# Kernel tuning notes

Measured on AMD Instinct MI355X. Metric: run time of the kernel, lower is better.

Reference implementation:

```python
import jax, jax.numpy as jnp
import numpy as np

B, N, FN, FE = 8, 256, 64, 64  # batch, nodes, node feat, edge feat


def gnn_layer(A, x, e, We, be, Wn, bn):
    # A: [B,N,N] float mask, x: [B,N,Fn], e: [B,N,N,Fe_in]
    b, n, fn = x.shape
    xi = jnp.broadcast_to(x[:, :, None, :], (b, n, n, fn))  # sender feats
    xj = jnp.broadcast_to(x[:, None, :, :], (b, n, n, fn))  # receiver feats
    h = jnp.concatenate([xi, xj, e], axis=-1)               # [B,N,N,2Fn+Fe]
    e_new = jax.nn.relu(jnp.einsum('bijk,kf->bijf', h, We) + be) * A[..., None]
    deg = jnp.clip(jnp.sum(A, axis=2), 1.0, None)           # [B,N]
    agg = jnp.sum(e_new, axis=2) / deg[..., None]           # mean over neighbors
    x_new = jax.nn.relu(jnp.concatenate([x, agg], axis=-1) @ Wn + bn)
    return x_new, e_new


def setup_inputs() -> dict:
    key = jax.random.key(0)
    ks = jax.random.split(key, 20)
    s = 0.05
    inp = {
        'edge_index': jax.random.randint(ks[0], (B, N, N), 0, 2, dtype=jnp.int32),
        'x': jax.random.normal(ks[1], (B, N, FN), dtype=jnp.float32),
        'edge_attr': jax.random.normal(ks[2], (B, N, N, FE), dtype=jnp.float32),
    }
    # 3 GNN layers: edge-update MLP (2Fn+Fe -> Fe) and node-update (Fn+Fe -> Fn)
    for l in range(3):
        inp[f'We{l}'] = jax.random.normal(ks[3 + 4 * l], (2 * FN + FE, FE), jnp.float32) * s
        inp[f'be{l}'] = jnp.zeros((FE,), jnp.float32)
        inp[f'Wn{l}'] = jax.random.normal(ks[4 + 4 * l], (FN + FE, FN), jnp.float32) * s
        inp[f'bn{l}'] = jnp.zeros((FN,), jnp.float32)
    # spectral-norm MLP head: Fe -> Fe -> Fe -> 1
    inp['W1'] = jax.random.normal(ks[15], (FE, FE), jnp.float32) * s
    inp['b1'] = jnp.zeros((FE,), jnp.float32)
    inp['W2'] = jax.random.normal(ks[16], (FE, FE), jnp.float32) * s
    inp['b2'] = jnp.zeros((FE,), jnp.float32)
    inp['W3'] = jax.random.normal(ks[17], (FE, 1), jnp.float32) * s
    inp['b3'] = jnp.zeros((1,), jnp.float32)
    return inp


def reference(edge_index, x, edge_attr,
              We0, be0, Wn0, bn0,
              We1, be1, Wn1, bn1,
              We2, be2, Wn2, bn2,
              W1, b1, W2, b2, W3, b3):
    A = edge_index.astype(jnp.float32)
    x = x.astype(jnp.float32)
    # layer 0 updates both nodes and edges
    x1, e = gnn_layer(A, x, edge_attr, We0, be0, Wn0, bn0)
    # middle layer(s): node output discarded (as in original forward)
    _, e = gnn_layer(A, x1, e, We1, be1, Wn1, bn1)
    # last layer
    _, edges = gnn_layer(A, x1, e, We2, be2, Wn2, bn2)
    # end == 'edge_mean'
    v = jnp.mean(edges, axis=(1, 2))  # [B, FE]
    h = jax.nn.relu(v @ W1 + b1)
    h = jax.nn.relu(h @ W2 + b2)
    out = h @ W3 + b3                  # [B, 1]
    return jnp.squeeze(out, axis=-1)   # [B]
```

## Files before the change

kernel.cpp:

```cpp
#include <hip/hip_runtime.h>

#define BB 8
#define NN 256
#define FF 64

typedef float f32x4 __attribute__((ext_vector_type(4)));
typedef short s16x8 __attribute__((ext_vector_type(8)));
typedef unsigned short u16;

#define MFMA_BF16(a, b, c) __builtin_amdgcn_mfma_f32_16x16x32_bf16(a, b, c, 0, 0, 0)

__device__ inline u16 f2bf(float x) {
    unsigned u = __float_as_uint(x);
    u += 0x7FFFu + ((u >> 16) & 1u);
    return (u16)(u >> 16);
}
__device__ inline float bf2f(u16 h) { return __uint_as_float(((unsigned)h) << 16); }

__device__ inline s16x8 cvt_a(float4 v0, float4 v1) {
    s16x8 a;
    a[0] = (short)f2bf(v0.x); a[1] = (short)f2bf(v0.y);
    a[2] = (short)f2bf(v0.z); a[3] = (short)f2bf(v0.w);
    a[4] = (short)f2bf(v1.x); a[5] = (short)f2bf(v1.y);
    a[6] = (short)f2bf(v1.z); a[7] = (short)f2bf(v1.w);
    return a;
}

__global__ __launch_bounds__(256) void wprep_kernel(
    const float* __restrict__ We0, const float* __restrict__ We1,
    const float* __restrict__ We2, u16* __restrict__ wimg)
{
    const float* src =
        (blockIdx.x == 0 ? We0 : (blockIdx.x == 1 ? We1 : We2)) + 2 * FF * FF;
    u16* hi = wimg + blockIdx.x * 8192;
    u16* lo = hi + 4096;
    for (int idx = threadIdx.x; idx < 4096; idx += 256) {
        const int f = idx >> 6, rem = idx & 63, cs = rem >> 3, j = rem & 7;
        const int k = ((cs ^ (f & 7)) << 3) | j;
        const float wv = src[k * FF + f];
        const u16 h = f2bf(wv);
        hi[idx] = h;
        lo[idx] = f2bf(wv - bf2f(h));
    }
}

__global__ __launch_bounds__(256) void pq_kernel(
    const float* __restrict__ x, const float* __restrict__ We,
    const float* __restrict__ be, float* __restrict__ P, float* __restrict__ Q,
    float* __restrict__ agg)
{
    const int rl = threadIdx.x >> 6, f = threadIdx.x & 63;
    const int r = blockIdx.x * 4 + rl;
    __shared__ float xs[4][FF];
    xs[rl][f] = x[r * FF + f];
    agg[r * FF + f] = 0.f;
    __syncthreads();
    float p = be[f], q = 0.f;
#pragma unroll
    for (int k = 0; k < FF; ++k) {
        const float xv = xs[rl][k];
        p = fmaf(xv, We[k * FF + f], p);
        q = fmaf(xv, We[(FF + k) * FF + f], q);
    }
    P[r * FF + f] = p;
    Q[r * FF + f] = q;
}

__global__ __launch_bounds__(256) void edge0_kernel(
    const float* __restrict__ e_in, const u16* __restrict__ whi,
    const u16* __restrict__ wlo, const float* __restrict__ P,
    const float* __restrict__ Q, const int* __restrict__ A,
    float* __restrict__ e_out, float* __restrict__ agg)
{
    __shared__ u16 Whl[4096], Wll[4096];
    __shared__ float Al[128], Pl[64];

    const int tid = threadIdx.x;
    const int bt  = blockIdx.x;
    const int bi  = bt >> 1;
    const int b   = bi >> 8;
    const int j0  = (bt & 1) << 7;

#pragma unroll
    for (int m = 0; m < 2; ++m) {
        ((uint4*)Whl)[tid + 256 * m] = ((const uint4*)whi)[tid + 256 * m];
        ((uint4*)Wll)[tid + 256 * m] = ((const uint4*)wlo)[tid + 256 * m];
    }
    if (tid < 128) Al[tid] = (float)A[bi * NN + j0 + tid];
    if (tid < 64)  Pl[tid] = P[bi * FF + tid];

    const int w = tid >> 6, lane = tid & 63;
    const int quad = lane >> 4, l15 = lane & 15, l7 = lane & 7;
    const int e_base = 32 * w;

    const float* erow = e_in + ((size_t)bi * NN + j0) * FF;

    s16x8 afr[2][2];
#pragma unroll
    for (int ks = 0; ks < 2; ++ks)
#pragma unroll
        for (int et = 0; et < 2; ++et) {
            const float* p = erow + (e_base + et * 16 + l15) * FF + ks * 32 + quad * 8;
            afr[ks][et] = cvt_a(*(const float4*)p, *(const float4*)(p + 4));
        }

    float qv[2][4][4];
    const float* Qb = Q + (size_t)b * NN * FF;
#pragma unroll
    for (int et = 0; et < 2; ++et)
#pragma unroll
        for (int ft = 0; ft < 4; ++ft)
#pragma unroll
            for (int r = 0; r < 4; ++r)
                qv[et][ft][r] =
                    Qb[(j0 + e_base + et * 16 + quad * 4 + r) * FF + ft * 16 + l15];

    __syncthreads();

    f32x4 acc[2][4];
#pragma unroll
    for (int et = 0; et < 2; ++et)
#pragma unroll
        for (int ft = 0; ft < 4; ++ft) acc[et][ft] = (f32x4){0.f, 0.f, 0.f, 0.f};

#pragma unroll
    for (int ks = 0; ks < 2; ++ks)
#pragma unroll
        for (int ft = 0; ft < 4; ++ft) {
            const int f  = ft * 16 + l15;
            const int ca = (ks * 4 + quad) ^ l7;
            const s16x8 bh = *(const s16x8*)&Whl[f * 64 + ca * 8];
            const s16x8 bl = *(const s16x8*)&Wll[f * 64 + ca * 8];
#pragma unroll
            for (int et = 0; et < 2; ++et) {
                acc[et][ft] = MFMA_BF16(afr[ks][et], bh, acc[et][ft]);
                acc[et][ft] = MFMA_BF16(afr[ks][et], bl, acc[et][ft]);
            }
        }

    float psum[4] = {0.f, 0.f, 0.f, 0.f};
#pragma unroll
    for (int et = 0; et < 2; ++et)
#pragma unroll
        for (int ft = 0; ft < 4; ++ft)
#pragma unroll
            for (int r = 0; r < 4; ++r) {
                const int el = e_base + et * 16 + quad * 4 + r;
                const int f  = ft * 16 + l15;
                const float val = acc[et][ft][r] + Pl[f] + qv[et][ft][r];
                const float rv  = fmaxf(val, 0.f) * Al[el];
                e_out[((size_t)bi * NN + j0 + el) * FF + f] = rv;
                psum[ft] += rv;
            }
#pragma unroll
    for (int ft = 0; ft < 4; ++ft) {
        psum[ft] += __shfl_down(psum[ft], 32);
        psum[ft] += __shfl_down(psum[ft], 16);
    }
    if (lane < 16) {
#pragma unroll
        for (int ft = 0; ft < 4; ++ft)
            atomicAdd(&agg[bi * FF + ft * 16 + l15], psum[ft]);
    }
}

__global__ __launch_bounds__(256) void nodepq_kernel(
    const float* __restrict__ x, const float* __restrict__ agg,
    const int* __restrict__ A,
    const float* __restrict__ Wn, const float* __restrict__ bn,
    const float* __restrict__ We1, const float* __restrict__ be1,
    const float* __restrict__ We2, const float* __restrict__ be2,
    float* __restrict__ P1, float* __restrict__ Q1,
    float* __restrict__ P2, float* __restrict__ Q2, float* __restrict__ v)
{
    const int rl = threadIdx.x >> 6, f = threadIdx.x & 63;
    const int r = blockIdx.x * 4 + rl;
    __shared__ float s[4][2 * FF];
    __shared__ float x1s[4][FF];

    float da = (float)A[r * NN + f] + (float)A[r * NN + f + 64] +
               (float)A[r * NN + f + 128] + (float)A[r * NN + f + 192];
#pragma unroll
    for (int off = 32; off > 0; off >>= 1) da += __shfl_down(da, off, 64);
    const float deg = fmaxf(__shfl(da, 0, 64), 1.0f);

    s[rl][f]      = x[r * FF + f];
    s[rl][FF + f] = agg[r * FF + f] / deg;
    if (blockIdx.x == 0) {
        v[threadIdx.x] = 0.f;
        v[256 + threadIdx.x] = 0.f;
    }
    __syncthreads();
    float a = bn[f];
#pragma unroll
    for (int k = 0; k < 2 * FF; ++k) a = fmaf(s[rl][k], Wn[k * FF + f], a);
    x1s[rl][f] = fmaxf(a, 0.f);
    __syncthreads();
    float p1 = be1[f], q1 = 0.f, p2 = be2[f], q2 = 0.f;
#pragma unroll
    for (int k = 0; k < FF; ++k) {
        const float xv = x1s[rl][k];
        p1 = fmaf(xv, We1[k * FF + f], p1);
        q1 = fmaf(xv, We1[(FF + k) * FF + f], q1);
        p2 = fmaf(xv, We2[k * FF + f], p2);
        q2 = fmaf(xv, We2[(FF + k) * FF + f], q2);
    }
    P1[r * FF + f] = p1;  Q1[r * FF + f] = q1;
    P2[r * FF + f] = p2;  Q2[r * FF + f] = q2;
}

__global__ __launch_bounds__(256) void edge12_kernel(
    const float* __restrict__ e_in,
    const u16* __restrict__ w1hi, const u16* __restrict__ w1lo,
    const u16* __restrict__ w2hi, const u16* __restrict__ w2lo,
    const float* __restrict__ P1, const float* __restrict__ Q1,
    const float* __restrict__ P2, const float* __restrict__ Q2,
    const int* __restrict__ A, float* __restrict__ v)
{
    __shared__ u16 W1h[4096], W1l[4096], W2h[4096], W2l[4096];
    __shared__ u16 E2[128 * 64];
    __shared__ float Al[128], Pl1[64], Pl2[64], red[64];

    const int tid = threadIdx.x;
    const int bt  = blockIdx.x;
    const int bi  = bt >> 1;
    const int b   = bi >> 8;
    const int j0  = (bt & 1) << 7;

#pragma unroll
    for (int m = 0; m < 2; ++m) {
        ((uint4*)W1h)[tid + 256 * m] = ((const uint4*)w1hi)[tid + 256 * m];
        ((uint4*)W1l)[tid + 256 * m] = ((const uint4*)w1lo)[tid + 256 * m];
        ((uint4*)W2h)[tid + 256 * m] = ((const uint4*)w2hi)[tid + 256 * m];
        ((uint4*)W2l)[tid + 256 * m] = ((const uint4*)w2lo)[tid + 256 * m];
    }
    if (tid < 128) Al[tid] = (float)A[bi * NN + j0 + tid];
    if (tid < 64) {
        Pl1[tid] = P1[bi * FF + tid];
        Pl2[tid] = P2[bi * FF + tid];
        red[tid] = 0.f;
    }

    const int w = tid >> 6, lane = tid & 63;
    const int quad = lane >> 4, l15 = lane & 15, l7 = lane & 7;
    const int e_base = 32 * w;

    const float* erow = e_in + ((size_t)bi * NN + j0) * FF;

    s16x8 afr[2][2];
#pragma unroll
    for (int ks = 0; ks < 2; ++ks)
#pragma unroll
        for (int et = 0; et < 2; ++et) {
            const float* p = erow + (e_base + et * 16 + l15) * FF + ks * 32 + quad * 8;
            afr[ks][et] = cvt_a(*(const float4*)p, *(const float4*)(p + 4));
        }

    float qv[2][4][4];
    {
        const float* Q1b = Q1 + (size_t)b * NN * FF;
#pragma unroll
        for (int et = 0; et < 2; ++et)
#pragma unroll
            for (int ft = 0; ft < 4; ++ft)
#pragma unroll
                for (int r = 0; r < 4; ++r)
                    qv[et][ft][r] =
                        Q1b[(j0 + e_base + et * 16 + quad * 4 + r) * FF + ft * 16 + l15];
    }

    __syncthreads();

    f32x4 acc[2][4];
#pragma unroll
    for (int et = 0; et < 2; ++et)
#pragma unroll
        for (int ft = 0; ft < 4; ++ft) acc[et][ft] = (f32x4){0.f, 0.f, 0.f, 0.f};

#pragma unroll
    for (int ks = 0; ks < 2; ++ks)
#pragma unroll
        for (int ft = 0; ft < 4; ++ft) {
            const int f  = ft * 16 + l15;
            const int ca = (ks * 4 + quad) ^ l7;
            const s16x8 bh = *(const s16x8*)&W1h[f * 64 + ca * 8];
            const s16x8 bl = *(const s16x8*)&W1l[f * 64 + ca * 8];
#pragma unroll
            for (int et = 0; et < 2; ++et) {
                acc[et][ft] = MFMA_BF16(afr[ks][et], bh, acc[et][ft]);
                acc[et][ft] = MFMA_BF16(afr[ks][et], bl, acc[et][ft]);
            }
        }

#pragma unroll
    for (int et = 0; et < 2; ++et)
#pragma unroll
        for (int ft = 0; ft < 4; ++ft)
#pragma unroll
            for (int r = 0; r < 4; ++r) {
                const int el = e_base + et * 16 + quad * 4 + r;
                const int f  = ft * 16 + l15;
                const float val = acc[et][ft][r] + Pl1[f] + qv[et][ft][r];
                const float rv  = fmaxf(val, 0.f) * Al[el];
                const int c  = f >> 3;
                const int cs = c ^ (el & 7);
                E2[el * 64 + cs * 8 + l7] = f2bf(rv);
            }

    {
        const float* Q2b = Q2 + (size_t)b * NN * FF;
#pragma unroll
        for (int et = 0; et < 2; ++et)
#pragma unroll
            for (int ft = 0; ft < 4; ++ft)
#pragma unroll
                for (int r = 0; r < 4; ++r)
                    qv[et][ft][r] =
                        Q2b[(j0 + e_base + et * 16 + quad * 4 + r) * FF + ft * 16 + l15];
    }

    __syncthreads();

#pragma unroll
    for (int et = 0; et < 2; ++et)
#pragma unroll
        for (int ft = 0; ft < 4; ++ft) acc[et][ft] = (f32x4){0.f, 0.f, 0.f, 0.f};

#pragma unroll
    for (int ks = 0; ks < 2; ++ks) {
        s16x8 a2[2];
#pragma unroll
        for (int et = 0; et < 2; ++et) {
            const int e  = e_base + et * 16 + l15;
            const int ca = (ks * 4 + quad) ^ l7;
            a2[et] = *(const s16x8*)&E2[e * 64 + ca * 8];
        }
#pragma unroll
        for (int ft = 0; ft < 4; ++ft) {
            const int f  = ft * 16 + l15;
            const int ca = (ks * 4 + quad) ^ l7;
            const s16x8 bh = *(const s16x8*)&W2h[f * 64 + ca * 8];
            const s16x8 bl = *(const s16x8*)&W2l[f * 64 + ca * 8];
#pragma unroll
            for (int et = 0; et < 2; ++et) {
                acc[et][ft] = MFMA_BF16(a2[et], bh, acc[et][ft]);
                acc[et][ft] = MFMA_BF16(a2[et], bl, acc[et][ft]);
            }
        }
    }

    float psum[4] = {0.f, 0.f, 0.f, 0.f};
#pragma unroll
    for (int et = 0; et < 2; ++et)
#pragma unroll
        for (int ft = 0; ft < 4; ++ft)
#pragma unroll
            for (int r = 0; r < 4; ++r) {
                const int el = e_base + et * 16 + quad * 4 + r;
                const int f  = ft * 16 + l15;
                const float val = acc[et][ft][r] + Pl2[f] + qv[et][ft][r];
                psum[ft] += fmaxf(val, 0.f) * Al[el];
            }
#pragma unroll
    for (int ft = 0; ft < 4; ++ft) {
        psum[ft] += __shfl_down(psum[ft], 32);
        psum[ft] += __shfl_down(psum[ft], 16);
    }
    if (lane < 16) {
#pragma unroll
        for (int ft = 0; ft < 4; ++ft)
            atomicAdd(&red[ft * 16 + l15], psum[ft]);
    }
    __syncthreads();
    if (tid < 64) atomicAdd(&v[b * FF + tid], red[tid]);
}

__global__ __launch_bounds__(64) void head_kernel(
    const float* __restrict__ vsum, const float* __restrict__ W1,
    const float* __restrict__ b1, const float* __restrict__ W2,
    const float* __restrict__ b2, const float* __restrict__ W3,
    const float* __restrict__ b3, float* __restrict__ out)
{
    const int f = threadIdx.x;
    __shared__ float hv[BB][FF];
    __shared__ float h1[BB][FF];
#pragma unroll
    for (int b = 0; b < BB; ++b) hv[b][f] = vsum[b * FF + f] * (1.0f / 65536.0f);
    __syncthreads();
#pragma unroll
    for (int b = 0; b < BB; ++b) {
        float acc = b1[f];
#pragma unroll
        for (int k = 0; k < FF; ++k) acc = fmaf(hv[b][k], W1[k * FF + f], acc);
        h1[b][f] = fmaxf(acc, 0.f);
    }
    __syncthreads();
#pragma unroll
    for (int b = 0; b < BB; ++b) {
        float acc = b2[f];
#pragma unroll
        for (int k = 0; k < FF; ++k) acc = fmaf(h1[b][k], W2[k * FF + f], acc);
        hv[b][f] = fmaxf(acc, 0.f);
    }
    __syncthreads();
#pragma unroll
    for (int b = 0; b < BB; ++b) {
        float p = hv[b][f] * W3[f];
#pragma unroll
        for (int off = 32; off > 0; off >>= 1) p += __shfl_down(p, off);
        if (f == 0) out[b] = p + b3[0];
    }
}

extern "C" void kernel_launch(void* const* d_in, const int* in_sizes, int n_in,
                              void* d_out, int out_size, void* d_ws, size_t ws_size,
                              hipStream_t stream)
{
    const int*   A      = (const int*)d_in[0];
    const float* x      = (const float*)d_in[1];
    float*       e_attr = (float*)d_in[2];

    const float* We0 = (const float*)d_in[3];
    const float* be0 = (const float*)d_in[4];
    const float* Wn0 = (const float*)d_in[5];
    const float* bn0 = (const float*)d_in[6];
    const float* We1 = (const float*)d_in[7];
    const float* be1 = (const float*)d_in[8];
    const float* We2 = (const float*)d_in[11];
    const float* be2 = (const float*)d_in[12];
    const float* W1 = (const float*)d_in[15];
    const float* b1 = (const float*)d_in[16];
    const float* W2 = (const float*)d_in[17];
    const float* b2 = (const float*)d_in[18];
    const float* W3 = (const float*)d_in[19];
    const float* b3 = (const float*)d_in[20];
    float* out = (float*)d_out;
    (void)in_sizes; (void)n_in; (void)out_size; (void)ws_size;

    const int R = BB * NN;
    float* P1  = (float*)d_ws;
    float* Q1  = P1 + R * FF;
    float* P2  = Q1 + R * FF;
    float* Q2  = P2 + R * FF;
    float* agg = Q2 + R * FF;
    float* v   = agg + R * FF;
    u16*  wimg = (u16*)(v + 512);

    const int EB = 2 * R;

    wprep_kernel<<<3, 256, 0, stream>>>(We0, We1, We2, wimg);
    pq_kernel<<<R / 4, 256, 0, stream>>>(x, We0, be0, P1, Q1, agg);
    edge0_kernel<<<EB, 256, 0, stream>>>(e_attr, wimg, wimg + 4096, P1, Q1, A,
                                         e_attr, agg);
    nodepq_kernel<<<R / 4, 256, 0, stream>>>(x, agg, A, Wn0, bn0, We1, be1,
                                             We2, be2, P1, Q1, P2, Q2, v);
    edge12_kernel<<<EB, 256, 0, stream>>>(e_attr,
                                          wimg + 8192, wimg + 12288,
                                          wimg + 16384, wimg + 20480,
                                          P1, Q1, P2, Q2, A, v);
    head_kernel<<<1, 64, 0, stream>>>(v, W1, b1, W2, b2, W3, b3, out);
}
```

Measured before the change: 361.7 us.

## Store intermediate edges as bf16, batch edge tiles per block, fold weight prep into pq

Layer-0 edge outputs are now written as bf16 into the existing edge buffer, reusing the same 256-byte row stride. edge12 reads these bf16 values directly as MFMA operands, which cuts the global traffic for the intermediate edge tensor roughly in half and removes an fp32-to-bf16 conversion. Each block now handles several edge tiles (T0/T12), so the LDS weight image is loaded fewer times. The MFMA operands are swapped so each lane holds four contiguous features, which allows vectorized P/Q loads and ushort4 stores. The weight-prep kernel is merged into pq_kernel to save a launch, edge12 uses a per-warp E2 buffer so block syncs are no longer needed, and atomics are accumulated across the tiles before they are issued. The risk is that the weight image from pq blocks 0-2 must be ready before edge0 runs, which holds because of stream order.

New measurement: 485.9 us. +34.3%, slower.

```diff
diff --git a/kernel.cpp b/kernel.cpp
--- a/kernel.cpp
+++ b/kernel.cpp
@@ -3,6 +3,9 @@
 #define BB 8
 #define NN 256
 #define FF 64
+#define T0  4
+#define T12 4
+#define E2S 72
 
 typedef float f32x4 __attribute__((ext_vector_type(4)));
 typedef short s16x8 __attribute__((ext_vector_type(8)));
@@ -17,43 +20,42 @@
 }
 __device__ inline float bf2f(u16 h) { return __uint_as_float(((unsigned)h) << 16); }
 
-__device__ inline s16x8 cvt_a(float4 v0, float4 v1) {
-    s16x8 a;
-    a[0] = (short)f2bf(v0.x); a[1] = (short)f2bf(v0.y);
-    a[2] = (short)f2bf(v0.z); a[3] = (short)f2bf(v0.w);
-    a[4] = (short)f2bf(v1.x); a[5] = (short)f2bf(v1.y);
-    a[6] = (short)f2bf(v1.z); a[7] = (short)f2bf(v1.w);
-    return a;
-}
-
-__global__ __launch_bounds__(256) void wprep_kernel(
-    const float* __restrict__ We0, const float* __restrict__ We1,
-    const float* __restrict__ We2, u16* __restrict__ wimg)
-{
-    const float* src =
-        (blockIdx.x == 0 ? We0 : (blockIdx.x == 1 ? We1 : We2)) + 2 * FF * FF;
-    u16* hi = wimg + blockIdx.x * 8192;
-    u16* lo = hi + 4096;
-    for (int idx = threadIdx.x; idx < 4096; idx += 256) {
-        const int f = idx >> 6, rem = idx & 63, cs = rem >> 3, j = rem & 7;
-        const int k = ((cs ^ (f & 7)) << 3) | j;
-        const float wv = src[k * FF + f];
-        const u16 h = f2bf(wv);
-        hi[idx] = h;
-        lo[idx] = f2bf(wv - bf2f(h));
-    }
+__device__ inline s16x8 cvt8(f32x4 a, f32x4 b) {
+    s16x8 r;
+    r[0] = (short)f2bf(a[0]); r[1] = (short)f2bf(a[1]);
+    r[2] = (short)f2bf(a[2]); r[3] = (short)f2bf(a[3]);
+    r[4] = (short)f2bf(b[0]); r[5] = (short)f2bf(b[1]);
+    r[6] = (short)f2bf(b[2]); r[7] = (short)f2bf(b[3]);
+    return r;
 }
 
 __global__ __launch_bounds__(256) void pq_kernel(
     const float* __restrict__ x, const float* __restrict__ We,
     const float* __restrict__ be, float* __restrict__ P, float* __restrict__ Q,
-    float* __restrict__ agg)
+    float* __restrict__ agg,
+    const float* __restrict__ We0, const float* __restrict__ We1,
+    const float* __restrict__ We2, u16* __restrict__ wimg)
 {
     const int rl = threadIdx.x >> 6, f = threadIdx.x & 63;
     const int r = blockIdx.x * 4 + rl;
     __shared__ float xs[4][FF];
     xs[rl][f] = x[r * FF + f];
     agg[r * FF + f] = 0.f;
+
+    if (blockIdx.x < 3) {
+        const float* src =
+            (blockIdx.x == 0 ? We0 : (blockIdx.x == 1 ? We1 : We2)) + 2 * FF * FF;
+        u16* hi = wimg + blockIdx.x * 8192;
+        u16* lo = hi + 4096;
+        for (int idx = threadIdx.x; idx < 4096; idx += 256) {
+            const int ff = idx >> 6, rem = idx & 63, cs = rem >> 3, j = rem & 7;
+            const int k = ((cs ^ (ff & 7)) << 3) | j;
+            const float wv = src[k * FF + ff];
+            const u16 h = f2bf(wv);
+            hi[idx] = h;
+            lo[idx] = f2bf(wv - bf2f(h));
+        }
+    }
     __syncthreads();
     float p = be[f], q = 0.f;
 #pragma unroll
@@ -67,100 +69,117 @@
 }
 
 __global__ __launch_bounds__(256) void edge0_kernel(
-    const float* __restrict__ e_in, const u16* __restrict__ whi,
-    const u16* __restrict__ wlo, const float* __restrict__ P,
-    const float* __restrict__ Q, const int* __restrict__ A,
-    float* __restrict__ e_out, float* __restrict__ agg)
-{
-    __shared__ u16 Whl[4096], Wll[4096];
-    __shared__ float Al[128], Pl[64];
-
+    const float* __restrict__ e_in, u16* __restrict__ e1_out,
+    const u16* __restrict__ wimg, const float* __restrict__ P,
+    const float* __restrict__ Q, const int* __restrict__ Adj,
+    float* __restrict__ agg)
+{
+    __shared__ u16 Wh[4096], Wl[4096];
     const int tid = threadIdx.x;
-    const int bt  = blockIdx.x;
-    const int bi  = bt >> 1;
-    const int b   = bi >> 8;
-    const int j0  = (bt & 1) << 7;
-
 #pragma unroll
     for (int m = 0; m < 2; ++m) {
-        ((uint4*)Whl)[tid + 256 * m] = ((const uint4*)whi)[tid + 256 * m];
-        ((uint4*)Wll)[tid + 256 * m] = ((const uint4*)wlo)[tid + 256 * m];
-    }
-    if (tid < 128) Al[tid] = (float)A[bi * NN + j0 + tid];
-    if (tid < 64)  Pl[tid] = P[bi * FF + tid];
+        ((uint4*)Wh)[tid + 256 * m] = ((const uint4*)wimg)[tid + 256 * m];
+        ((uint4*)Wl)[tid + 256 * m] = ((const uint4*)(wimg + 4096))[tid + 256 * m];
+    }
+    __syncthreads();
 
     const int w = tid >> 6, lane = tid & 63;
     const int quad = lane >> 4, l15 = lane & 15, l7 = lane & 7;
-    const int e_base = 32 * w;
-
-    const float* erow = e_in + ((size_t)bi * NN + j0) * FF;
-
-    s16x8 afr[2][2];
-#pragma unroll
-    for (int ks = 0; ks < 2; ++ks)
+    const int e0 = 32 * w + l15;
+
+#pragma unroll
+    for (int tt = 0; tt < T0; ++tt) {
+        const int bt = blockIdx.x * T0 + tt;
+        const int bi = bt >> 1, b = bi >> 8;
+        const int j0 = (bt & 1) << 7;
+
+        f32x4 ef[2][2][2];
+        const float* erow = e_in + ((size_t)bi * NN + j0) * FF;
+#pragma unroll
+        for (int ks = 0; ks < 2; ++ks)
+#pragma unroll
+            for (int et = 0; et < 2; ++et) {
+                const float* p = erow + (size_t)(e0 + 16 * et) * FF + ks * 32 + quad * 8;
+                ef[ks][et][0] = *(const f32x4*)p;
+                ef[ks][et][1] = *(const f32x4*)(p + 4);
+            }
+
+        float av[2];
+#pragma unroll
+        for (int et = 0; et < 2; ++et)
+            av[et] = (float)Adj[bi * NN + j0 + e0 + 16 * et];
+        f32x4 pv[4];
+#pragma unroll
+        for (int ft = 0; ft < 4; ++ft)
+            pv[ft] = *(const f32x4*)(P + bi * FF + ft * 16 + quad * 4);
+        f32x4 qv[2][4];
+        const float* Qb = Q + ((size_t)b * NN + j0) * FF;
+#pragma unroll
+        for (int et = 0; et < 2; ++et)
+#pragma unroll
+            for (int ft = 0; ft < 4; ++ft)
+                qv[et][ft] = *(const f32x4*)(Qb + (size_t)(e0 + 16 * et) * FF +
+                                             ft * 16 + quad * 4);
+
+        f32x4 acc[2][4];
+#pragma unroll
+        for (int et = 0; et < 2; ++et)
+#pragma unroll
+            for (int ft = 0; ft < 4; ++ft) acc[et][ft] = (f32x4){0.f, 0.f, 0.f, 0.f};
+
+#pragma unroll
+        for (int ks = 0; ks < 2; ++ks) {
+            s16x8 efr[2];
+#pragma unroll
+            for (int et = 0; et < 2; ++et) efr[et] = cvt8(ef[ks][et][0], ef[ks][et][1]);
+#pragma unroll
+            for (int ft = 0; ft < 4; ++ft) {
+                const int off = (16 * ft + l15) * 64 + (((ks * 4 + quad) ^ l7) << 3);
+                const s16x8 ah = *(const s16x8*)&Wh[off];
+                const s16x8 al = *(const s16x8*)&Wl[off];
+#pragma unroll
+                for (int et = 0; et < 2; ++et) {
+                    acc[et][ft] = MFMA_BF16(ah, efr[et], acc[et][ft]);
+                    acc[et][ft] = MFMA_BF16(al, efr[et], acc[et][ft]);
+                }
+            }
+        }
+
+        float sac[4][4];
+#pragma unroll
+        for (int ft = 0; ft < 4; ++ft)
+#pragma unroll
+            for (int r = 0; r < 4; ++r) sac[ft][r] = 0.f;
 #pragma unroll
         for (int et = 0; et < 2; ++et) {
-            const float* p = erow + (e_base + et * 16 + l15) * FF + ks * 32 + quad * 8;
-            afr[ks][et] = cvt_a(*(const float4*)p, *(const float4*)(p + 4));
-        }
-
-    float qv[2][4][4];
-    const float* Qb = Q + (size_t)b * NN * FF;
-#pragma unroll
-    for (int et = 0; et < 2; ++et)
+            const size_t erow_g = (size_t)bi * NN + j0 + e0 + 16 * et;
+#pragma unroll
+            for (int ft = 0; ft < 4; ++ft) {
+                float rr[4];
+#pragma unroll
+                for (int r = 0; r < 4; ++r) {
+                    const float val = acc[et][ft][r] + pv[ft][r] + qv[et][ft][r];
+                    rr[r] = fmaxf(val, 0.f) * av[et];
+                    sac[ft][r] += rr[r];
+                }
+                ushort4 st;
+                st.x = f2bf(rr[0]); st.y = f2bf(rr[1]);
+                st.z = f2bf(rr[2]); st.w = f2bf(rr[3]);
+                *(ushort4*)(e1_out + erow_g * 128 + ft * 16 + quad * 4) = st;
+            }
+        }
 #pragma unroll
         for (int ft = 0; ft < 4; ++ft)
 #pragma unroll
-            for (int r = 0; r < 4; ++r)
-                qv[et][ft][r] =
-                    Qb[(j0 + e_base + et * 16 + quad * 4 + r) * FF + ft * 16 + l15];
-
-    __syncthreads();
-
-    f32x4 acc[2][4];
-#pragma unroll
-    for (int et = 0; et < 2; ++et)
-#pragma unroll
-        for (int ft = 0; ft < 4; ++ft) acc[et][ft] = (f32x4){0.f, 0.f, 0.f, 0.f};
-
-#pragma unroll
-    for (int ks = 0; ks < 2; ++ks)
-#pragma unroll
-        for (int ft = 0; ft < 4; ++ft) {
-            const int f  = ft * 16 + l15;
-            const int ca = (ks * 4 + quad) ^ l7;
-            const s16x8 bh = *(const s16x8*)&Whl[f * 64 + ca * 8];
-            const s16x8 bl = *(const s16x8*)&Wll[f * 64 + ca * 8];
-#pragma unroll
-            for (int et = 0; et < 2; ++et) {
-                acc[et][ft] = MFMA_BF16(afr[ks][et], bh, acc[et][ft]);
-                acc[et][ft] = MFMA_BF16(afr[ks][et], bl, acc[et][ft]);
-            }
-        }
-
-    float psum[4] = {0.f, 0.f, 0.f, 0.f};
-#pragma unroll
-    for (int et = 0; et < 2; ++et)
-#pragma unroll
-        for (int ft = 0; ft < 4; ++ft)
-#pragma unroll
             for (int r = 0; r < 4; ++r) {
-                const int el = e_base + et * 16 + quad * 4 + r;
-                const int f  = ft * 16 + l15;
-                const float val = acc[et][ft][r] + Pl[f] + qv[et][ft][r];
-                const float rv  = fmaxf(val, 0.f) * Al[el];
-                e_out[((size_t)bi * NN + j0 + el) * FF + f] = rv;
-                psum[ft] += rv;
-            }
-#pragma unroll
-    for (int ft = 0; ft < 4; ++ft) {
-        psum[ft] += __shfl_down(psum[ft], 32);
-        psum[ft] += __shfl_down(psum[ft], 16);
-    }
-    if (lane < 16) {
-#pragma unroll
-        for (int ft = 0; ft < 4; ++ft)
-            atomicAdd(&agg[bi * FF + ft * 16 + l15], psum[ft]);
+                float s = sac[ft][r];
+                s += __shfl_xor(s, 1, 16);
+                s += __shfl_xor(s, 2, 16);
+                s += __shfl_xor(s, 4, 16);
+                s += __shfl_xor(s, 8, 16);
+                if (l15 == 0)
+                    atomicAdd(&agg[bi * FF + ft * 16 + quad * 4 + r], s);
+            }
     }
 }
 
@@ -210,169 +229,161 @@
 }
 
 __global__ __launch_bounds__(256) void edge12_kernel(
-    const float* __restrict__ e_in,
-    const u16* __restrict__ w1hi, const u16* __restrict__ w1lo,
-    const u16* __restrict__ w2hi, const u16* __restrict__ w2lo,
+    const u16* __restrict__ e1,
+    const u16* __restrict__ w1img, const u16* __restrict__ w2img,
     const float* __restrict__ P1, const float* __restrict__ Q1,
     const float* __restrict__ P2, const float* __restrict__ Q2,
-    const int* __restrict__ A, float* __restrict__ v)
+    const int* __restrict__ Adj, float* __restrict__ v)
 {
     __shared__ u16 W1h[4096], W1l[4096], W2h[4096], W2l[4096];
-    __shared__ u16 E2[128 * 64];
-    __shared__ float Al[128], Pl1[64], Pl2[64], red[64];
-
+    __shared__ u16 E2[4][32 * E2S];
     const int tid = threadIdx.x;
-    const int bt  = blockIdx.x;
-    const int bi  = bt >> 1;
-    const int b   = bi >> 8;
-    const int j0  = (bt & 1) << 7;
-
 #pragma unroll
     for (int m = 0; m < 2; ++m) {
-        ((uint4*)W1h)[tid + 256 * m] = ((const uint4*)w1hi)[tid + 256 * m];
-        ((uint4*)W1l)[tid + 256 * m] = ((const uint4*)w1lo)[tid + 256 * m];
-        ((uint4*)W2h)[tid + 256 * m] = ((const uint4*)w2hi)[tid + 256 * m];
-        ((uint4*)W2l)[tid + 256 * m] = ((const uint4*)w2lo)[tid + 256 * m];
-    }
-    if (tid < 128) Al[tid] = (float)A[bi * NN + j0 + tid];
-    if (tid < 64) {
-        Pl1[tid] = P1[bi * FF + tid];
-        Pl2[tid] = P2[bi * FF + tid];
-        red[tid] = 0.f;
-    }
+        ((uint4*)W1h)[tid + 256 * m] = ((const uint4*)w1img)[tid + 256 * m];
+        ((uint4*)W1l)[tid + 256 * m] = ((const uint4*)(w1img + 4096))[tid + 256 * m];
+        ((uint4*)W2h)[tid + 256 * m] = ((const uint4*)w2img)[tid + 256 * m];
+        ((uint4*)W2l)[tid + 256 * m] = ((const uint4*)(w2img + 4096))[tid + 256 * m];
+    }
+    __syncthreads();
 
     const int w = tid >> 6, lane = tid & 63;
     const int quad = lane >> 4, l15 = lane & 15, l7 = lane & 7;
-    const int e_base = 32 * w;
-
-    const float* erow = e_in + ((size_t)bi * NN + j0) * FF;
-
-    s16x8 afr[2][2];
-#pragma unroll
-    for (int ks = 0; ks < 2; ++ks)
+    const int e0 = 32 * w + l15;
+    u16* E2w = E2[w];
+    const int b = (blockIdx.x * T12) >> 9;
+
+    float vac[4][4];
+#pragma unroll
+    for (int ft = 0; ft < 4; ++ft)
+#pragma unroll
+        for (int r = 0; r < 4; ++r) vac[ft][r] = 0.f;
+
+#pragma unroll
+    for (int tt = 0; tt < T12; ++tt) {
+        const int bt = blockIdx.x * T12 + tt;
+        const int bi = bt >> 1;
+        const int j0 = (bt & 1) << 7;
+
+        s16x8 bfr[2][2];
+#pragma unroll
+        for (int ks = 0; ks < 2; ++ks)
+#pragma unroll
+            for (int et = 0; et < 2; ++et)
+                bfr[ks][et] = *(const s16x8*)(e1 +
+                    ((size_t)bi * NN + j0 + e0 + 16 * et) * 128 + ks * 32 + quad * 8);
+
+        float av[2];
+#pragma unroll
+        for (int et = 0; et < 2; ++et)
+            av[et] = (float)Adj[bi * NN + j0 + e0 + 16 * et];
+        f32x4 pv[4];
+#pragma unroll
+        for (int ft = 0; ft < 4; ++ft)
+            pv[ft] = *(const f32x4*)(P1 + bi * FF + ft * 16 + quad * 4);
+        f32x4 qv[2][4];
+        const float* Q1b = Q1 + ((size_t)b * NN + j0) * FF;
+#pragma unroll
+        for (int et = 0; et < 2; ++et)
+#pragma unroll
+            for (int ft = 0; ft < 4; ++ft)
+                qv[et][ft] = *(const f32x4*)(Q1b + (size_t)(e0 + 16 * et) * FF +
+                                             ft * 16 + quad * 4);
+
+        f32x4 acc[2][4];
+#pragma unroll
+        for (int et = 0; et < 2; ++et)
+#pragma unroll
+            for (int ft = 0; ft < 4; ++ft) acc[et][ft] = (f32x4){0.f, 0.f, 0.f, 0.f};
+#pragma unroll
+        for (int ks = 0; ks < 2; ++ks)
+#pragma unroll
+            for (int ft = 0; ft < 4; ++ft) {
+                const int off = (16 * ft + l15) * 64 + (((ks * 4 + quad) ^ l7) << 3);
+                const s16x8 ah = *(const s16x8*)&W1h[off];
+                const s16x8 al = *(const s16x8*)&W1l[off];
+#pragma unroll
+                for (int et = 0; et < 2; ++et) {
+                    acc[et][ft] = MFMA_BF16(ah, bfr[ks][et], acc[et][ft]);
+                    acc[et][ft] = MFMA_BF16(al, bfr[ks][et], acc[et][ft]);
+                }
+            }
+
 #pragma unroll
         for (int et = 0; et < 2; ++et) {
-            const float* p = erow + (e_base + et * 16 + l15) * FF + ks * 32 + quad * 8;
-            afr[ks][et] = cvt_a(*(const float4*)p, *(const float4*)(p + 4));
-        }
-
-    float qv[2][4][4];
-    {
-        const float* Q1b = Q1 + (size_t)b * NN * FF;
+            const int erow_l = (16 * et + l15) * E2S;
+#pragma unroll
+            for (int ft = 0; ft < 4; ++ft) {
+                float rr[4];
+#pragma unroll
+                for (int r = 0; r < 4; ++r) {
+                    const float val = acc[et][ft][r] + pv[ft][r] + qv[et][ft][r];
+                    rr[r] = fmaxf(val, 0.f) * av[et];
+                }
+                ushort4 st;
+                st.x = f2bf(rr[0]); st.y = f2bf(rr[1]);
+                st.z = f2bf(rr[2]); st.w = f2bf(rr[3]);
+                *(ushort4*)&E2w[erow_l + ft * 16 + quad * 4] = st;
+            }
+        }
+
+#pragma unroll
+        for (int ft = 0; ft < 4; ++ft)
+            pv[ft] = *(const f32x4*)(P2 + bi * FF + ft * 16 + quad * 4);
+        const float* Q2b = Q2 + ((size_t)b * NN + j0) * FF;
 #pragma unroll
         for (int et = 0; et < 2; ++et)
 #pragma unroll
             for (int ft = 0; ft < 4; ++ft)
-#pragma unroll
-                for (int r = 0; r < 4; ++r)
-                    qv[et][ft][r] =
-                        Q1b[(j0 + e_base + et * 16 + quad * 4 + r) * FF + ft * 16 + l15];
-    }
-
-    __syncthreads();
-
-    f32x4 acc[2][4];
-#pragma unroll
-    for (int et = 0; et < 2; ++et)
-#pragma unroll
-        for (int ft = 0; ft < 4; ++ft) acc[et][ft] = (f32x4){0.f, 0.f, 0.f, 0.f};
-
-#pragma unroll
-    for (int ks = 0; ks < 2; ++ks)
-#pragma unroll
-        for (int ft = 0; ft < 4; ++ft) {
-            const int f  = ft * 16 + l15;
-            const int ca = (ks * 4 + quad) ^ l7;
-            const s16x8 bh = *(const s16x8*)&W1h[f * 64 + ca * 8];
-            const s16x8 bl = *(const s16x8*)&W1l[f * 64 + ca * 8];
-#pragma unroll
-            for (int et = 0; et < 2; ++et) {
-                acc[et][ft] = MFMA_BF16(afr[ks][et], bh, acc[et][ft]);
-                acc[et][ft] = MFMA_BF16(afr[ks][et], bl, acc[et][ft]);
-            }
-        }
-
-#pragma unroll
-    for (int et = 0; et < 2; ++et)
-#pragma unroll
-        for (int ft = 0; ft < 4; ++ft)
-#pragma unroll
-            for (int r = 0; r < 4; ++r) {
-                const int el = e_base + et * 16 + quad * 4 + r;
-                const int f  = ft * 16 + l15;
-                const float val = acc[et][ft][r] + Pl1[f] + qv[et][ft][r];
-                const float rv  = fmaxf(val, 0.f) * Al[el];
-                const int c  = f >> 3;
-                const int cs = c ^ (el & 7);
-                E2[el * 64 + cs * 8 + l7] = f2bf(rv);
-            }
-
-    {
-        const float* Q2b = Q2 + (size_t)b * NN * FF;
+                qv[et][ft] = *(const f32x4*)(Q2b + (size_t)(e0 + 16 * et) * FF +
+                                             ft * 16 + quad * 4);
+
+#pragma unroll
+        for (int et = 0; et < 2; ++et)
+#pragma unroll
+            for (int ft = 0; ft < 4; ++ft) acc[et][ft] = (f32x4){0.f, 0.f, 0.f, 0.f};
+#pragma unroll
+        for (int ks = 0; ks < 2; ++ks) {
+            s16x8 e2f[2];
+#pragma unroll
+            for (int et = 0; et < 2; ++et)
+                e2f[et] = *(const s16x8*)&E2w[(16 * et + l15) * E2S + ks * 32 + quad * 8];
+#pragma unroll
+            for (int ft = 0; ft < 4; ++ft) {
+                const int off = (16 * ft + l15) * 64 + (((ks * 4 + quad) ^ l7) << 3);
+                const s16x8 ah = *(const s16x8*)&W2h[off];
+                const s16x8 al = *(const s16x8*)&W2l[off];
+#pragma unroll
+                for (int et = 0; et < 2; ++et) {
+                    acc[et][ft] = MFMA_BF16(ah, e2f[et], acc[et][ft]);
+                    acc[et][ft] = MFMA_BF16(al, e2f[et], acc[et][ft]);
+                }
+            }
+        }
+
 #pragma unroll
         for (int et = 0; et < 2; ++et)
 #pragma unroll
             for (int ft = 0; ft < 4; ++ft)
 #pragma unroll
-                for (int r = 0; r < 4; ++r)
-                    qv[et][ft][r] =
-                        Q2b[(j0 + e_base + et * 16 + quad * 4 + r) * FF + ft * 16 + l15];
-    }
-
-    __syncthreads();
-
-#pragma unroll
-    for (int et = 0; et < 2; ++et)
-#pragma unroll
-        for (int ft = 0; ft < 4; ++ft) acc[et][ft] = (f32x4){0.f, 0.f, 0.f, 0.f};
-
-#pragma unroll
-    for (int ks = 0; ks < 2; ++ks) {
-        s16x8 a2[2];
-#pragma unroll
-        for (int et = 0; et < 2; ++et) {
-            const int e  = e_base + et * 16 + l15;
-            const int ca = (ks * 4 + quad) ^ l7;
-            a2[et] = *(const s16x8*)&E2[e * 64 + ca * 8];
-        }
-#pragma unroll
-        for (int ft = 0; ft < 4; ++ft) {
-            const int f  = ft * 16 + l15;
-            const int ca = (ks * 4 + quad) ^ l7;
-            const s16x8 bh = *(const s16x8*)&W2h[f * 64 + ca * 8];
-            const s16x8 bl = *(const s16x8*)&W2l[f * 64 + ca * 8];
-#pragma unroll
-            for (int et = 0; et < 2; ++et) {
-                acc[et][ft] = MFMA_BF16(a2[et], bh, acc[et][ft]);
-                acc[et][ft] = MFMA_BF16(a2[et], bl, acc[et][ft]);
-            }
-        }
-    }
-
-    float psum[4] = {0.f, 0.f, 0.f, 0.f};
-#pragma unroll
-    for (int et = 0; et < 2; ++et)
-#pragma unroll
-        for (int ft = 0; ft < 4; ++ft)
-#pragma unroll
-            for (int r = 0; r < 4; ++r) {
-                const int el = e_base + et * 16 + quad * 4 + r;
-                const int f  = ft * 16 + l15;
-                const float val = acc[et][ft][r] + Pl2[f] + qv[et][ft][r];
-                psum[ft] += fmaxf(val, 0.f) * Al[el];
-            }
-#pragma unroll
-    for (int ft = 0; ft < 4; ++ft) {
-        psum[ft] += __shfl_down(psum[ft], 32);
-        psum[ft] += __shfl_down(psum[ft], 16);
-    }
-    if (lane < 16) {
-#pragma unroll
-        for (int ft = 0; ft < 4; ++ft)
-            atomicAdd(&red[ft * 16 + l15], psum[ft]);
-    }
-    __syncthreads();
-    if (tid < 64) atomicAdd(&v[b * FF + tid], red[tid]);
+                for (int r = 0; r < 4; ++r) {
+                    const float val = acc[et][ft][r] + pv[ft][r] + qv[et][ft][r];
+                    vac[ft][r] += fmaxf(val, 0.f) * av[et];
+                }
+    }
+
+#pragma unroll
+    for (int ft = 0; ft < 4; ++ft)
+#pragma unroll
+        for (int r = 0; r < 4; ++r) {
+            float s = vac[ft][r];
+            s += __shfl_xor(s, 1, 16);
+            s += __shfl_xor(s, 2, 16);
+            s += __shfl_xor(s, 4, 16);
+            s += __shfl_xor(s, 8, 16);
+            if (l15 == 0)
+                atomicAdd(&v[b * FF + ft * 16 + quad * 4 + r], s);
+        }
 }
 
 __global__ __launch_bounds__(64) void head_kernel(
@@ -446,17 +457,14 @@
     float* v   = agg + R * FF;
     u16*  wimg = (u16*)(v + 512);
 
-    const int EB = 2 * R;
-
-    wprep_kernel<<<3, 256, 0, stream>>>(We0, We1, We2, wimg);
-    pq_kernel<<<R / 4, 256, 0, stream>>>(x, We0, be0, P1, Q1, agg);
-    edge0_kernel<<<EB, 256, 0, stream>>>(e_attr, wimg, wimg + 4096, P1, Q1, A,
-                                         e_attr, agg);
+    u16* e1 = (u16*)e_attr;
+
+    pq_kernel<<<R / 4, 256, 0, stream>>>(x, We0, be0, P1, Q1, agg,
+                                         We0, We1, We2, wimg);
+    edge0_kernel<<<2 * R / T0, 256, 0, stream>>>(e_attr, e1, wimg, P1, Q1, A, agg);
     nodepq_kernel<<<R / 4, 256, 0, stream>>>(x, agg, A, Wn0, bn0, We1, be1,
                                              We2, be2, P1, Q1, P2, Q2, v);
-    edge12_kernel<<<EB, 256, 0, stream>>>(e_attr,
-                                          wimg + 8192, wimg + 12288,
-                                          wimg + 16384, wimg + 20480,
-                                          P1, Q1, P2, Q2, A, v);
+    edge12_kernel<<<2 * R / T12, 256, 0, stream>>>(e1, wimg + 8192, wimg + 16384,
+                                                   P1, Q1, P2, Q2, A, v);
     head_kernel<<<1, 64, 0, stream>>>(v, W1, b1, W2, b2, W3, b3, out);
 }
```
